# Kernel tuning notes

Measured on AMD Instinct MI355X. Metric: run time of the kernel, lower is better.

The kernel has to match this reference:

```python
import jax, jax.numpy as jnp
import numpy as np

B, S, D, MULT, K, EPS = 8, 2048, 512, 4, 9, 1e-6


def setup_inputs() -> dict:
    key = jax.random.key(0)
    ks = jax.random.split(key, 12)
    w = lambda k, shape, s=0.02: jax.random.normal(k, shape, dtype=jnp.float32) * s
    return dict(
        x=jax.random.normal(ks[0], (B, S, D), dtype=jnp.float32),
        g=jnp.ones((D,), jnp.float32),
        W1=w(ks[1], (D, D)), b1=jnp.zeros((D,), jnp.float32),
        W2=w(ks[2], (D, D)), b2=jnp.zeros((D,), jnp.float32),
        dw_w=w(ks[3], (D, D, K)), dw_b=jnp.zeros((D,), jnp.float32),
        pw_w=w(ks[4], (D, D, 1)), pw_b=jnp.zeros((D,), jnp.float32),
        Wi=w(ks[5], (D, D)), bi=jnp.zeros((D,), jnp.float32),
        Wr=w(ks[6], (D, D)), br=jnp.zeros((D,), jnp.float32),
        lam=jax.random.normal(ks[7], (D,), dtype=jnp.float32),
        Wm1=w(ks[8], (D, D * MULT)), bm1=jnp.zeros((D * MULT,), jnp.float32),
        Wm2=w(ks[9], (D * MULT, D)), bm2=jnp.zeros((D,), jnp.float32),
    )


def _rglru(x, Wi, bi, Wr, br, lam):
    # Griffin RG-LRU: h_t = a_t * h_{t-1} + sqrt(1 - a_t^2) * (i_t * x_t), h_0 = 0
    r = jax.nn.sigmoid(x @ Wr + br)                 # [B,S,D] recurrence gate
    i = jax.nn.sigmoid(x @ Wi + bi)                 # [B,S,D] input gate
    log_a = -8.0 * jax.nn.softplus(lam) * r         # [B,S,D]
    a = jnp.exp(log_a)
    b = jnp.sqrt(1.0 - jnp.exp(2.0 * log_a)) * (i * x)

    def combine(e1, e2):
        a1, b1 = e1
        a2, b2 = e2
        return (a1 * a2, a2 * b1 + b2)

    _, h = jax.lax.associative_scan(combine, (a, b), axis=1)
    return h


def _conv1d(x_cdS, w_oik, b_o, pad):
    y = jax.lax.conv_general_dilated(
        x_cdS, w_oik, window_strides=(1,), padding=[pad],
        dimension_numbers=("NCH", "OIH", "NCH"))
    return y + b_o[None, :, None]


def reference(x, g, W1, b1, W2, b2, dw_w, dw_b, pw_w, pw_b,
              Wi, bi, Wr, br, lam, Wm1, bm1, Wm2, bm2):
    scale = jnp.sqrt(jnp.float32(D))

    def rms(t):  # matches torch: x / (||x||_2 + eps) * sqrt(D) * g
        n = jnp.linalg.norm(t, axis=-1, keepdims=True) + EPS
        return t / n * scale * g

    skip = x
    xn = rms(x)
    l1 = xn @ W1 + b1                               # [B,S,D]
    l2 = xn @ W2 + b2                               # [B,S,D]
    c = jnp.transpose(l1, (0, 2, 1))                # [B,D,S]
    c = _conv1d(c, dw_w, dw_b, (K // 2, K // 2))    # 'same' padding, k=9
    c = _conv1d(c, pw_w, pw_b, (0, 0))              # pointwise k=1
    l1 = jnp.transpose(c, (0, 2, 1))                # [B,S,D]
    l1 = _rglru(l1, Wi, bi, Wr, br, lam)
    x1 = l1 * jax.nn.gelu(l2, approximate=False) + skip

    skip2 = x1
    xn2 = rms(x1)
    h = xn2 @ Wm1 + bm1                             # [B,S,4D]
    out = (jax.nn.gelu(h, approximate=False) * h) @ Wm2 + bm2 + skip2
    return out
```

## Files before the change

### kernel.cpp

```cpp
#include <hip/hip_runtime.h>
#include <hip/hip_bf16.h>

typedef unsigned short ushort_t;
typedef unsigned short vus8 __attribute__((ext_vector_type(8)));
typedef short vs8 __attribute__((ext_vector_type(8)));
typedef float vf4 __attribute__((ext_vector_type(4)));

#define D_DIM 512
#define S_LEN 2048
#define B_SZ 8
#define T_TOK 16384
#define NCH 64
#define CLEN 32

__device__ __forceinline__ float bf2f(ushort_t u) {
  union { unsigned int i; float f; } v;
  v.i = ((unsigned int)u) << 16;
  return v.f;
}
__device__ __forceinline__ ushort_t f2bf(float f) {
  union { float f; unsigned int i; } v;
  v.f = f;
  unsigned int r = v.i + 0x7fffu + ((v.i >> 16) & 1u);
  return (ushort_t)(r >> 16);
}
__device__ __forceinline__ float gelu_exact(float x) {
  return 0.5f * x * (1.0f + erff(x * 0.7071067811865475f));
}
__device__ __forceinline__ float ld_in(const void* p, size_t i, int fl) {
  return fl ? ((const float*)p)[i] : bf2f(((const ushort_t*)p)[i]);
}
__device__ __forceinline__ void gld_lds16(const ushort_t* g, ushort_t* l) {
  __builtin_amdgcn_global_load_lds(
      (const __attribute__((address_space(1))) unsigned int*)g,
      (__attribute__((address_space(3))) unsigned int*)l, 16, 0, 0);
}

__device__ __forceinline__ void ab_compute(ushort_t rp, ushort_t ip, ushort_t xv,
                                           float sp8, float& a, float& b) {
  float r = 1.f / (1.f + expf(-bf2f(rp)));
  float ig = 1.f / (1.f + expf(-bf2f(ip)));
  float la = -sp8 * r;
  a = expf(la);
  b = sqrtf(fmaxf(0.f, -expm1f(2.f * la))) * ig * bf2f(xv);
}

__global__ void detect_flag(const void* g, int* flag) {
  const ushort_t* u = (const ushort_t*)g;
  flag[0] = (u[0] == 0x3F80 && u[1] == 0x3F80) ? 0 : 1;
  flag[1] = 0;
}

#define NJOBS 18
struct PrepJobs {
  const void* src[NJOBS];
  ushort_t* dst[NJOBS];
  int R[NJOBS];
  int C[NJOBS];
  int mode[NJOBS];
  int start[NJOBS];
  int njobs;
};
__global__ void mega_prep(PrepJobs J, const int* __restrict__ flag) {
  __shared__ ushort_t ts[32][33];
  int fl = *flag;
  int bid = blockIdx.x;
  int j = 0;
  while (j + 1 < J.njobs && bid >= J.start[j + 1]) j++;
  int tile = bid - J.start[j];
  const void* in = J.src[j];
  ushort_t* out = J.dst[j];
  int mode = J.mode[j];
  if (mode == 2) {
    int n = J.R[j];
    int base = tile * 8192;
#pragma unroll 4
    for (int q = 0; q < 32; q++) {
      int i = base + q * 256 + threadIdx.x;
      if (i < n) out[i] = fl ? f2bf(((const float*)in)[i]) : ((const ushort_t*)in)[i];
    }
    return;
  }
  int R = J.R[j], C = J.C[j];
  int tpr = C >> 5;
  int bc = tile % tpr, br = tile / tpr;
  int tx = threadIdx.x & 31, ty = threadIdx.x >> 5;
#pragma unroll
  for (int i = 0; i < 32; i += 8) {
    size_t idx = (size_t)(br * 32 + ty + i) * C + bc * 32 + tx;
    ts[ty + i][tx] = fl ? f2bf(((const float*)in)[idx]) : ((const ushort_t*)in)[idx];
  }
  __syncthreads();
#pragma unroll
  for (int i = 0; i < 32; i += 8) {
    int r = bc * 32 + ty + i;
    int orow = (mode == 1) ? (r % 9) * 512 + r / 9 : r;
    out[(size_t)orow * R + br * 32 + tx] = ts[tx][ty + i];
  }
}

__global__ void gam_kernel(const ushort_t* __restrict__ tpw, const ushort_t* __restrict__ dwbc,
                           const ushort_t* __restrict__ pwbc, float* __restrict__ gam) {
  int wave = threadIdx.x >> 6, lane = threadIdx.x & 63;
  int o = blockIdx.x * 4 + wave;
  vus8 v = *(const vus8*)(tpw + (size_t)o * 512 + lane * 8);
  vus8 w = *(const vus8*)(dwbc + lane * 8);
  float p = 0.f;
#pragma unroll
  for (int q = 0; q < 8; q++) p += bf2f(v[q]) * bf2f(w[q]);
#pragma unroll
  for (int off = 32; off; off >>= 1) p += __shfl_xor(p, off, 64);
  if (lane == 0) gam[o] = p + bf2f(pwbc[o]);
}

__global__ void rms_kernel(const void* __restrict__ x, const int* __restrict__ flag,
                           const ushort_t* __restrict__ gc, ushort_t* __restrict__ out) {
  int fl = *flag;
  int wave = threadIdx.x >> 6, lane = threadIdx.x & 63;
  int row = blockIdx.x * 4 + wave;
  size_t base = (size_t)row * D_DIM + lane * 8;
  float f[8];
  float ss = 0.f;
#pragma unroll
  for (int j = 0; j < 8; j++) { f[j] = ld_in(x, base + j, fl); ss += f[j] * f[j]; }
#pragma unroll
  for (int off = 32; off > 0; off >>= 1) ss += __shfl_xor(ss, off, 64);
  float sc = 22.62741699796952f / (sqrtf(ss) + 1e-6f);
  vus8 o;
#pragma unroll
  for (int j = 0; j < 8; j++) o[j] = f2bf(f[j] * sc * bf2f(gc[lane * 8 + j]));
  *(vus8*)(out + base) = o;
}

template <int ACT>
__global__ __launch_bounds__(256, 2) void gemm_bt(
    const ushort_t* __restrict__ A, const ushort_t* __restrict__ Bt,
    const ushort_t* __restrict__ bias, void* __restrict__ Cv,
    const ushort_t* __restrict__ skip, const int* __restrict__ outflag, int N, int K, int lda,
    int row0, size_t zsA, size_t zsB, size_t zsC) {
  __shared__ __align__(16) ushort_t As[128 * 32];
  __shared__ __align__(16) ushort_t Bs[128 * 32];
  A += (size_t)blockIdx.z * zsA;
  Bt += (size_t)blockIdx.z * zsB;
  const size_t zC = (size_t)blockIdx.z * zsC;
  const int tid = threadIdx.x;
  const int bm = blockIdx.y, bn = blockIdx.x;
  const int wave = tid >> 6, lane = tid & 63;
  const int wm = wave & 1, wn = wave >> 1;
  const int quad = lane >> 4, l16 = lane & 15;
  const int ofl = (ACT == 2) ? *outflag : 0;
  const int srow = wave * 32 + (lane >> 2);
  const int scol = (lane & 3) * 8;
  const ushort_t* gA = A + (size_t)(bm * 128 + srow) * lda + scol;
  const ushort_t* gB = Bt + (size_t)(bn * 128 + srow) * K + scol;
  ushort_t* lA0 = As + (wave * 32) * 32;
  ushort_t* lA1 = As + (wave * 32 + 16) * 32;
  ushort_t* lB0 = Bs + (wave * 32) * 32;
  ushort_t* lB1 = Bs + (wave * 32 + 16) * 32;
  vf4 acc[4][4] = {};
  for (int k0 = 0; k0 < K; k0 += 32) {
    __syncthreads();
    gld_lds16(gA + k0, lA0);
    gld_lds16(gA + k0 + (size_t)16 * lda, lA1);
    gld_lds16(gB + k0, lB0);
    gld_lds16(gB + k0 + (size_t)16 * K, lB1);
    __syncthreads();
    vs8 af[4], bfr[4];
#pragma unroll
    for (int mi = 0; mi < 4; mi++)
      af[mi] = *(const vs8*)(As + (wm * 64 + mi * 16 + l16) * 32 + quad * 8);
#pragma unroll
    for (int ni = 0; ni < 4; ni++)
      bfr[ni] = *(const vs8*)(Bs + (wn * 64 + ni * 16 + l16) * 32 + quad * 8);
#pragma unroll
    for (int mi = 0; mi < 4; mi++)
#pragma unroll
      for (int ni = 0; ni < 4; ni++)
        acc[mi][ni] =
            __builtin_amdgcn_mfma_f32_16x16x32_bf16(af[mi], bfr[ni], acc[mi][ni], 0, 0, 0);
  }
#pragma unroll
  for (int mi = 0; mi < 4; mi++) {
#pragma unroll
    for (int ni = 0; ni < 4; ni++) {
      int gcol = bn * 128 + wn * 64 + ni * 16 + l16;
      float bv = bias ? bf2f(bias[gcol]) : 0.f;
#pragma unroll
      for (int r = 0; r < 4; r++) {
        int grow = row0 + bm * 128 + wm * 64 + mi * 16 + quad * 4 + r;
        size_t oidx = zC + (size_t)grow * N + gcol;
        float v = acc[mi][ni][r] + bv;
        if (ACT == 1) v = gelu_exact(v) * v;
        if (ACT == 2) v += bf2f(skip[(size_t)grow * N + gcol]);
        if (ACT == 2 && ofl) ((float*)Cv)[oidx] = v;
        else ((ushort_t*)Cv)[oidx] = f2bf(v);
      }
    }
  }
}

#define LDA_CONV 1024
__global__ __launch_bounds__(256, 2) void conv_gemm(
    const ushort_t* __restrict__ A, const ushort_t* __restrict__ Bt9,
    const float* __restrict__ gam, ushort_t* __restrict__ C) {
  __shared__ __align__(16) ushort_t Ah[136 * 32];
  __shared__ __align__(16) ushort_t Bs[3 * 128 * 32];
  const int tid = threadIdx.x;
  const int bid = blockIdx.x;
  const int xid = bid & 7, cid = bid >> 3;
  const int bn = xid >> 1;
  const int bm = (xid & 1) * 64 + cid;
  const int wave = tid >> 6, lane = tid & 63;
  const int wm = wave & 1, wn = wave >> 1;
  const int quad = lane >> 4, l16 = lane & 15;
  const int pos = bm & 15;
  const bool first = (pos == 0), last = (pos == 15);
  const int blrow = lane >> 2;
  const int bscol = (lane & 3) * 8;
  vf4 acc[4][4] = {};
  for (int k0 = 0; k0 < D_DIM; k0 += 32) {
    __syncthreads();
    for (int c = tid; c < 544; c += 256) {
      int j = c >> 2, col = (c & 3) * 8;
      vus8 v = {0, 0, 0, 0, 0, 0, 0, 0};
      bool valid = !((first && j < 4) || (last && j >= 132));
      if (valid)
        v = *(const vus8*)(A + (size_t)(bm * 128 + j - 4) * LDA_CONV + k0 + col);
      *(vus8*)(Ah + j * 32 + col) = v;
    }
#pragma unroll
    for (int kg = 0; kg < 3; kg++) {
      if (kg) __syncthreads();
#pragma unroll
      for (int h = 0; h < 6; h++) {
        int m = h * 4 + wave;
        int r = m * 16 + blrow;
        int kbl = m >> 3;
        int ro = r & 127;
        const ushort_t* g = Bt9 + ((size_t)(kg * 3 + kbl) * D_DIM + bn * 128 + ro) * D_DIM +
                            k0 + bscol;
        gld_lds16(g, Bs + m * 16 * 32);
      }
      __syncthreads();
#pragma unroll
      for (int kbl = 0; kbl < 3; kbl++) {
        int kb = kg * 3 + kbl;
        vs8 af[4], bfr[4];
#pragma unroll
        for (int mi = 0; mi < 4; mi++)
          af[mi] = *(const vs8*)(Ah + (wm * 64 + mi * 16 + l16 + kb) * 32 + quad * 8);
#pragma unroll
        for (int ni = 0; ni < 4; ni++)
          bfr[ni] = *(const vs8*)(Bs + kbl * 4096 + (wn * 64 + ni * 16 + l16) * 32 + quad * 8);
#pragma unroll
        for (int mi = 0; mi < 4; mi++)
#pragma unroll
          for (int ni = 0; ni < 4; ni++)
            acc[mi][ni] =
                __builtin_amdgcn_mfma_f32_16x16x32_bf16(af[mi], bfr[ni], acc[mi][ni], 0, 0, 0);
      }
    }
  }
#pragma unroll
  for (int mi = 0; mi < 4; mi++) {
#pragma unroll
    for (int ni = 0; ni < 4; ni++) {
      int gcol = bn * 128 + wn * 64 + ni * 16 + l16;
      float gv = gam[gcol];
#pragma unroll
      for (int r = 0; r < 4; r++) {
        int grow = bm * 128 + wm * 64 + mi * 16 + quad * 4 + r;
        C[(size_t)grow * D_DIM + gcol] = f2bf(acc[mi][ni][r] + gv);
      }
    }
  }
}

__global__ void scan_pass1(const ushort_t* __restrict__ P, const ushort_t* __restrict__ xin,
                           const ushort_t* __restrict__ lamc, float* __restrict__ Aagg,
                           float* __restrict__ Bagg) {
  int bid = blockIdx.x;
  int dblk = bid & 1, c = (bid >> 1) & (NCH - 1), bb = bid >> 7;
  int d = dblk * 256 + threadIdx.x;
  float l = bf2f(lamc[d]);
  float sp8 = 8.f * ((l > 20.f) ? l : log1pf(expf(l)));
  size_t baseP = ((size_t)bb * S_LEN + c * CLEN) * 1024 + d;
  size_t baseX = ((size_t)bb * S_LEN + c * CLEN) * D_DIM + d;
  float Ap = 1.f, h = 0.f;
  for (int s = 0; s < CLEN; s++) {
    float av, bv;
    ab_compute(P[baseP + (size_t)s * 1024], P[baseP + 512 + (size_t)s * 1024],
               xin[baseX + (size_t)s * D_DIM], sp8, av, bv);
    Ap *= av;
    h = av * h + bv;
  }
  size_t o = ((size_t)bb * NCH + c) * D_DIM + d;
  Aagg[o] = Ap;
  Bagg[o] = h;
}

__global__ void scan_carry(const float* __restrict__ Aagg, const float* __restrict__ Bagg,
                           float* __restrict__ carry) {
  int idx = blockIdx.x * 256 + threadIdx.x;
  int bb = idx >> 9, d = idx & (D_DIM - 1);
  float h = 0.f;
  for (int c = 0; c < NCH; c++) {
    size_t o = ((size_t)bb * NCH + c) * D_DIM + d;
    carry[o] = h;
    h = Aagg[o] * h + Bagg[o];
  }
}

__global__ void scan_pass2(const ushort_t* __restrict__ P, const ushort_t* xin,
                           const ushort_t* __restrict__ lamc, const float* __restrict__ carry,
                           const ushort_t* __restrict__ P12, const void* __restrict__ x,
                           const int* __restrict__ flag, ushort_t* x1) {
  int fl = *flag;
  int bid = blockIdx.x;
  int dblk = bid & 1, c = (bid >> 1) & (NCH - 1), bb = bid >> 7;
  int d = dblk * 256 + threadIdx.x;
  float l = bf2f(lamc[d]);
  float sp8 = 8.f * ((l > 20.f) ? l : log1pf(expf(l)));
  float h = carry[((size_t)bb * NCH + c) * D_DIM + d];
  size_t baseP = ((size_t)bb * S_LEN + c * CLEN) * 1024 + d;
  size_t baseL = ((size_t)bb * S_LEN + c * CLEN) * 1024 + 512 + d;
  size_t base = ((size_t)bb * S_LEN + c * CLEN) * D_DIM + d;
  for (int s = 0; s < CLEN; s++) {
    size_t idx = base + (size_t)s * D_DIM;
    float av, bv;
    ab_compute(P[baseP + (size_t)s * 1024], P[baseP + 512 + (size_t)s * 1024], xin[idx], sp8,
               av, bv);
    h = av * h + bv;
    float l2v = bf2f(P12[baseL + (size_t)s * 1024]);
    float xv = ld_in(x, idx, fl);
    x1[idx] = f2bf(h * gelu_exact(l2v) + xv);
  }
}

extern "C" void kernel_launch(void* const* d_in, const int* in_sizes, int n_in, void* d_out,
                              int out_size, void* d_ws, size_t ws_size, hipStream_t stream) {
  (void)in_sizes; (void)n_in; (void)out_size; (void)ws_size;
  const void* x   = d_in[0];
  const void* g   = d_in[1];
  const void* W1  = d_in[2];
  const void* b1  = d_in[3];
  const void* W2  = d_in[4];
  const void* b2  = d_in[5];
  const void* dww = d_in[6];
  const void* dwb = d_in[7];
  const void* pww = d_in[8];
  const void* pwb = d_in[9];
  const void* Wi  = d_in[10];
  const void* bi  = d_in[11];
  const void* Wr  = d_in[12];
  const void* br  = d_in[13];
  const void* lam = d_in[14];
  const void* Wm1 = d_in[15];
  const void* bm1 = d_in[16];
  const void* Wm2 = d_in[17];
  const void* bm2 = d_in[18];

  char* ws = (char*)d_ws;
  size_t off = 0;
  auto take = [&](size_t n) {
    void* p = ws + off;
    off += (n + 255) & ~(size_t)255;
    return p;
  };
  const size_t ACT_B = (size_t)T_TOK * D_DIM * 2;
  int* flag = (int*)take(256);
  ushort_t* tW12 = (ushort_t*)take((size_t)1024 * 512 * 2);
  ushort_t* tWri = (ushort_t*)take((size_t)1024 * 512 * 2);
  ushort_t* tWm1 = (ushort_t*)take((size_t)2048 * 512 * 2);
  ushort_t* tWm2 = (ushort_t*)take((size_t)2048 * 512 * 2);
  ushort_t* Wp   = (ushort_t*)take((size_t)9 * 512 * 512 * 2);
  ushort_t* gc   = (ushort_t*)take(512 * 2);
  ushort_t* lamc = (ushort_t*)take(512 * 2);
  ushort_t* b12c = (ushort_t*)take(1024 * 2);
  ushort_t* bric = (ushort_t*)take(1024 * 2);
  ushort_t* bm2c = (ushort_t*)take(512 * 2);
  ushort_t* bm1c = (ushort_t*)take(2048 * 2);
  ushort_t* dwbc = (ushort_t*)take(512 * 2);
  ushort_t* pwbc = (ushort_t*)take(512 * 2);
  float* gam     = (float*)take(512 * 4);
  ushort_t* S0 = (ushort_t*)take(ACT_B);
  ushort_t* S1 = (ushort_t*)take(ACT_B);
  ushort_t* S2 = (ushort_t*)take(ACT_B);
  ushort_t* S3 = (ushort_t*)take(ACT_B);
  ushort_t* S4 = (ushort_t*)take(ACT_B);
  float* Aagg  = (float*)take((size_t)B_SZ * NCH * D_DIM * 4);
  float* Bagg  = (float*)take((size_t)B_SZ * NCH * D_DIM * 4);
  float* carry = (float*)take((size_t)B_SZ * NCH * D_DIM * 4);
  const int* zflag = flag + 1;
  ushort_t* tpw  = S2;
  ushort_t* tdwT = S3;
  ushort_t* P12  = S0;
  ushort_t* Pri  = S3;
  ushort_t* u2   = S0;

  detect_flag<<<1, 1, 0, stream>>>(g, flag);
  PrepJobs J;
  const void* js[NJOBS] = {g, lam, b1, b2, dwb, pwb, br, bi, bm2, bm1, pww,
                           W1, W2, Wr, Wi, Wm1, Wm2, dww};
  ushort_t* jd[NJOBS] = {gc, lamc, b12c, b12c + 512, dwbc, pwbc, bric, bric + 512, bm2c, bm1c,
                         tpw, tW12, tW12 + (size_t)512 * 512, tWri, tWri + (size_t)512 * 512,
                         tWm1, tWm2, tdwT};
  int jR[NJOBS] = {512, 512, 512, 512, 512, 512, 512, 512, 512, 2048, 262144,
                   512, 512, 512, 512, 512, 2048, 512};
  int jC[NJOBS] = {0, 0, 0, 0, 0, 0, 0, 0, 0, 0, 0, 512, 512, 512, 512, 2048, 512, 4608};
  int jm[NJOBS] = {2, 2, 2, 2, 2, 2, 2, 2, 2, 2, 2, 0, 0, 0, 0, 0, 0, 1};
  int cum = 0;
  for (int i = 0; i < NJOBS; i++) {
    J.src[i] = js[i]; J.dst[i] = jd[i]; J.R[i] = jR[i]; J.C[i] = jC[i]; J.mode[i] = jm[i];
    J.start[i] = cum;
    cum += (jm[i] == 2) ? (jR[i] + 8191) / 8192 : (jC[i] / 32) * (jR[i] / 32);
  }
  J.njobs = NJOBS;
  mega_prep<<<cum, 256, 0, stream>>>(J, flag);
  gemm_bt<0><<<dim3(4, 4, 9), 256, 0, stream>>>(tpw, tdwT, nullptr, Wp, nullptr, zflag, 512,
                                                512, 512, 0, 0, (size_t)512 * 512,
                                                (size_t)512 * 512);
  gam_kernel<<<128, 256, 0, stream>>>(tpw, dwbc, pwbc, gam);

  rms_kernel<<<T_TOK / 4, 256, 0, stream>>>(x, flag, gc, S4);
  gemm_bt<0><<<dim3(8, 128), 256, 0, stream>>>(S4, tW12, b12c, P12, nullptr, zflag, 1024, 512,
                                               512, 0, 0, 0, 0);
  conv_gemm<<<512, 256, 0, stream>>>(P12, Wp, gam, S2);
  gemm_bt<0><<<dim3(8, 128), 256, 0, stream>>>(S2, tWri, bric, Pri, nullptr, zflag, 1024, 512,
                                               512, 0, 0, 0, 0);
  scan_pass1<<<B_SZ * NCH * 2, 256, 0, stream>>>(Pri, S2, lamc, Aagg, Bagg);
  scan_carry<<<16, 256, 0, stream>>>(Aagg, Bagg, carry);
  scan_pass2<<<B_SZ * NCH * 2, 256, 0, stream>>>(Pri, S2, lamc, carry, P12, x, flag, S2);

  rms_kernel<<<T_TOK / 4, 256, 0, stream>>>(S2, zflag, gc, S4);
  for (int c = 0; c < 2; c++) {
    const ushort_t* xc = S4 + (size_t)c * 8192 * D_DIM;
    gemm_bt<1><<<dim3(16, 64), 256, 0, stream>>>(xc, tWm1, bm1c, u2, nullptr, zflag, 2048, 512,
                                                 512, 0, 0, 0, 0);
    gemm_bt<2><<<dim3(4, 64), 256, 0, stream>>>(u2, tWm2, bm2c, d_out, S2, flag, 512, 2048,
                                                2048, c * 8192, 0, 0, 0);
  }
}
```

Before: 566.2 us.

## Fold second RMSNorm into MLP GEMM epilogue and drop flag kernel

Removes the second rms_kernel pass. Row sum-of-squares is now accumulated with atomics inside scan_pass2, the gain vector is folded into Wm1 during weight prep, and the per-row scale is applied in a new GEMM epilogue before the GELU. It also drops the detect_flag launch by checking the input dtype inline, precomputes the softplus of lam once, and runs the MLP as two full-size GEMMs instead of two chunks. The cost is a memset plus per-row atomics in the scan, and applying the norm after the bf16 matmul rather than before it changes rounding slightly.

```diff
diff --git a/kernel.cpp b/kernel.cpp
--- a/kernel.cpp
+++ b/kernel.cpp
@@ -29,6 +29,9 @@
 }
 __device__ __forceinline__ float ld_in(const void* p, size_t i, int fl) {
   return fl ? ((const float*)p)[i] : bf2f(((const ushort_t*)p)[i]);
+}
+__device__ __forceinline__ int dt_fl(const ushort_t* gdt) {
+  return !(gdt[0] == 0x3F80 && gdt[1] == 0x3F80);
 }
 __device__ __forceinline__ void gld_lds16(const ushort_t* g, ushort_t* l) {
   __builtin_amdgcn_global_load_lds(
@@ -43,12 +46,6 @@
   float la = -sp8 * r;
   a = expf(la);
   b = sqrtf(fmaxf(0.f, -expm1f(2.f * la))) * ig * bf2f(xv);
-}
-
-__global__ void detect_flag(const void* g, int* flag) {
-  const ushort_t* u = (const ushort_t*)g;
-  flag[0] = (u[0] == 0x3F80 && u[1] == 0x3F80) ? 0 : 1;
-  flag[1] = 0;
 }
 
 #define NJOBS 18
@@ -59,11 +56,12 @@
   int C[NJOBS];
   int mode[NJOBS];
   int start[NJOBS];
+  const void* gsrc;
   int njobs;
 };
-__global__ void mega_prep(PrepJobs J, const int* __restrict__ flag) {
+__global__ void mega_prep(PrepJobs J, const ushort_t* __restrict__ gdt) {
   __shared__ ushort_t ts[32][33];
-  int fl = *flag;
+  int fl = dt_fl(gdt);
   int bid = blockIdx.x;
   int j = 0;
   while (j + 1 < J.njobs && bid >= J.start[j + 1]) j++;
@@ -95,12 +93,23 @@
   for (int i = 0; i < 32; i += 8) {
     int r = bc * 32 + ty + i;
     int orow = (mode == 1) ? (r % 9) * 512 + r / 9 : r;
-    out[(size_t)orow * R + br * 32 + tx] = ts[tx][ty + i];
+    ushort_t val = ts[tx][ty + i];
+    if (mode == 3) {
+      int kcol = br * 32 + tx;
+      val = f2bf(bf2f(val) * ld_in(J.gsrc, kcol, fl));
+    }
+    out[(size_t)orow * R + br * 32 + tx] = val;
   }
 }
 
 __global__ void gam_kernel(const ushort_t* __restrict__ tpw, const ushort_t* __restrict__ dwbc,
-                           const ushort_t* __restrict__ pwbc, float* __restrict__ gam) {
+                           const ushort_t* __restrict__ pwbc, const ushort_t* __restrict__ lamc,
+                           float* __restrict__ gam, float* __restrict__ sp8b) {
+  int t = blockIdx.x * 256 + threadIdx.x;
+  if (t < 512) {
+    float l = bf2f(lamc[t]);
+    sp8b[t] = 8.f * ((l > 20.f) ? l : log1pf(expf(l)));
+  }
   int wave = threadIdx.x >> 6, lane = threadIdx.x & 63;
   int o = blockIdx.x * 4 + wave;
   vus8 v = *(const vus8*)(tpw + (size_t)o * 512 + lane * 8);
@@ -113,9 +122,9 @@
   if (lane == 0) gam[o] = p + bf2f(pwbc[o]);
 }
 
-__global__ void rms_kernel(const void* __restrict__ x, const int* __restrict__ flag,
+__global__ void rms_kernel(const void* __restrict__ x, const ushort_t* __restrict__ gdt,
                            const ushort_t* __restrict__ gc, ushort_t* __restrict__ out) {
-  int fl = *flag;
+  int fl = dt_fl(gdt);
   int wave = threadIdx.x >> 6, lane = threadIdx.x & 63;
   int row = blockIdx.x * 4 + wave;
   size_t base = (size_t)row * D_DIM + lane * 8;
@@ -136,8 +145,9 @@
 __global__ __launch_bounds__(256, 2) void gemm_bt(
     const ushort_t* __restrict__ A, const ushort_t* __restrict__ Bt,
     const ushort_t* __restrict__ bias, void* __restrict__ Cv,
-    const ushort_t* __restrict__ skip, const int* __restrict__ outflag, int N, int K, int lda,
-    int row0, size_t zsA, size_t zsB, size_t zsC) {
+    const ushort_t* __restrict__ skip, const float* __restrict__ rowss,
+    const ushort_t* __restrict__ gdt, int N, int K, int lda, int row0,
+    size_t zsA, size_t zsB, size_t zsC) {
   __shared__ __align__(16) ushort_t As[128 * 32];
   __shared__ __align__(16) ushort_t Bs[128 * 32];
   A += (size_t)blockIdx.z * zsA;
@@ -148,7 +158,7 @@
   const int wave = tid >> 6, lane = tid & 63;
   const int wm = wave & 1, wn = wave >> 1;
   const int quad = lane >> 4, l16 = lane & 15;
-  const int ofl = (ACT == 2) ? *outflag : 0;
+  const int ofl = (ACT == 2) ? dt_fl(gdt) : 0;
   const int srow = wave * 32 + (lane >> 2);
   const int scol = (lane & 3) * 8;
   const ushort_t* gA = A + (size_t)(bm * 128 + srow) * lda + scol;
@@ -189,8 +199,14 @@
       for (int r = 0; r < 4; r++) {
         int grow = row0 + bm * 128 + wm * 64 + mi * 16 + quad * 4 + r;
         size_t oidx = zC + (size_t)grow * N + gcol;
-        float v = acc[mi][ni][r] + bv;
-        if (ACT == 1) v = gelu_exact(v) * v;
+        float v;
+        if (ACT == 3) {
+          float sc = 22.62741699796952f / (sqrtf(rowss[grow]) + 1e-6f);
+          v = acc[mi][ni][r] * sc + bv;
+          v = gelu_exact(v) * v;
+        } else {
+          v = acc[mi][ni][r] + bv;
+        }
         if (ACT == 2) v += bf2f(skip[(size_t)grow * N + gcol]);
         if (ACT == 2 && ofl) ((float*)Cv)[oidx] = v;
         else ((ushort_t*)Cv)[oidx] = f2bf(v);
@@ -277,13 +293,12 @@
 }
 
 __global__ void scan_pass1(const ushort_t* __restrict__ P, const ushort_t* __restrict__ xin,
-                           const ushort_t* __restrict__ lamc, float* __restrict__ Aagg,
+                           const float* __restrict__ sp8b, float* __restrict__ Aagg,
                            float* __restrict__ Bagg) {
   int bid = blockIdx.x;
   int dblk = bid & 1, c = (bid >> 1) & (NCH - 1), bb = bid >> 7;
   int d = dblk * 256 + threadIdx.x;
-  float l = bf2f(lamc[d]);
-  float sp8 = 8.f * ((l > 20.f) ? l : log1pf(expf(l)));
+  float sp8 = sp8b[d];
   size_t baseP = ((size_t)bb * S_LEN + c * CLEN) * 1024 + d;
   size_t baseX = ((size_t)bb * S_LEN + c * CLEN) * D_DIM + d;
   float Ap = 1.f, h = 0.f;
@@ -311,29 +326,35 @@
   }
 }
 
-__global__ void scan_pass2(const ushort_t* __restrict__ P, const ushort_t* xin,
-                           const ushort_t* __restrict__ lamc, const float* __restrict__ carry,
-                           const ushort_t* __restrict__ P12, const void* __restrict__ x,
-                           const int* __restrict__ flag, ushort_t* x1) {
-  int fl = *flag;
+__global__ void scan_pass2(const ushort_t* __restrict__ P, const float* __restrict__ sp8b,
+                           const float* __restrict__ carry, const ushort_t* __restrict__ P12,
+                           const void* __restrict__ x, const ushort_t* __restrict__ gdt,
+                           ushort_t* xio, float* __restrict__ rowss) {
+  int fl = dt_fl(gdt);
   int bid = blockIdx.x;
   int dblk = bid & 1, c = (bid >> 1) & (NCH - 1), bb = bid >> 7;
   int d = dblk * 256 + threadIdx.x;
-  float l = bf2f(lamc[d]);
-  float sp8 = 8.f * ((l > 20.f) ? l : log1pf(expf(l)));
+  int lane = threadIdx.x & 63;
+  float sp8 = sp8b[d];
   float h = carry[((size_t)bb * NCH + c) * D_DIM + d];
   size_t baseP = ((size_t)bb * S_LEN + c * CLEN) * 1024 + d;
   size_t baseL = ((size_t)bb * S_LEN + c * CLEN) * 1024 + 512 + d;
   size_t base = ((size_t)bb * S_LEN + c * CLEN) * D_DIM + d;
+  int row0 = bb * S_LEN + c * CLEN;
   for (int s = 0; s < CLEN; s++) {
     size_t idx = base + (size_t)s * D_DIM;
     float av, bv;
-    ab_compute(P[baseP + (size_t)s * 1024], P[baseP + 512 + (size_t)s * 1024], xin[idx], sp8,
+    ab_compute(P[baseP + (size_t)s * 1024], P[baseP + 512 + (size_t)s * 1024], xio[idx], sp8,
                av, bv);
     h = av * h + bv;
     float l2v = bf2f(P12[baseL + (size_t)s * 1024]);
     float xv = ld_in(x, idx, fl);
-    x1[idx] = f2bf(h * gelu_exact(l2v) + xv);
+    float v = h * gelu_exact(l2v) + xv;
+    xio[idx] = f2bf(v);
+    float p = v * v;
+#pragma unroll
+    for (int o2 = 32; o2; o2 >>= 1) p += __shfl_xor(p, o2, 64);
+    if (lane == 0) atomicAdd(&rowss[row0 + s], p);
   }
 }
 
@@ -359,6 +380,7 @@
   const void* bm1 = d_in[16];
   const void* Wm2 = d_in[17];
   const void* bm2 = d_in[18];
+  const ushort_t* gdt = (const ushort_t*)g;
 
   char* ws = (char*)d_ws;
   size_t off = 0;
@@ -368,7 +390,6 @@
     return p;
   };
   const size_t ACT_B = (size_t)T_TOK * D_DIM * 2;
-  int* flag = (int*)take(256);
   ushort_t* tW12 = (ushort_t*)take((size_t)1024 * 512 * 2);
   ushort_t* tWri = (ushort_t*)take((size_t)1024 * 512 * 2);
   ushort_t* tWm1 = (ushort_t*)take((size_t)2048 * 512 * 2);
@@ -383,6 +404,8 @@
   ushort_t* dwbc = (ushort_t*)take(512 * 2);
   ushort_t* pwbc = (ushort_t*)take(512 * 2);
   float* gam     = (float*)take(512 * 4);
+  float* sp8b    = (float*)take(512 * 4);
+  float* rowss   = (float*)take((size_t)T_TOK * 4);
   ushort_t* S0 = (ushort_t*)take(ACT_B);
   ushort_t* S1 = (ushort_t*)take(ACT_B);
   ushort_t* S2 = (ushort_t*)take(ACT_B);
@@ -391,14 +414,14 @@
   float* Aagg  = (float*)take((size_t)B_SZ * NCH * D_DIM * 4);
   float* Bagg  = (float*)take((size_t)B_SZ * NCH * D_DIM * 4);
   float* carry = (float*)take((size_t)B_SZ * NCH * D_DIM * 4);
-  const int* zflag = flag + 1;
-  ushort_t* tpw  = S2;
-  ushort_t* tdwT = S3;
-  ushort_t* P12  = S0;
-  ushort_t* Pri  = S3;
-  ushort_t* u2   = S0;
-
-  detect_flag<<<1, 1, 0, stream>>>(g, flag);
+  ushort_t* tpw  = S0;
+  ushort_t* tdwT = S1;
+  ushort_t* Pri  = S0;
+  ushort_t* P12  = S2;
+  ushort_t* u    = S0;
+
+  hipMemsetAsync(rowss, 0, (size_t)T_TOK * 4, stream);
+
   PrepJobs J;
   const void* js[NJOBS] = {g, lam, b1, b2, dwb, pwb, br, bi, bm2, bm1, pww,
                            W1, W2, Wr, Wi, Wm1, Wm2, dww};
@@ -408,36 +431,33 @@
   int jR[NJOBS] = {512, 512, 512, 512, 512, 512, 512, 512, 512, 2048, 262144,
                    512, 512, 512, 512, 512, 2048, 512};
   int jC[NJOBS] = {0, 0, 0, 0, 0, 0, 0, 0, 0, 0, 0, 512, 512, 512, 512, 2048, 512, 4608};
-  int jm[NJOBS] = {2, 2, 2, 2, 2, 2, 2, 2, 2, 2, 2, 0, 0, 0, 0, 0, 0, 1};
+  int jm[NJOBS] = {2, 2, 2, 2, 2, 2, 2, 2, 2, 2, 2, 0, 0, 0, 0, 3, 0, 1};
   int cum = 0;
   for (int i = 0; i < NJOBS; i++) {
     J.src[i] = js[i]; J.dst[i] = jd[i]; J.R[i] = jR[i]; J.C[i] = jC[i]; J.mode[i] = jm[i];
     J.start[i] = cum;
     cum += (jm[i] == 2) ? (jR[i] + 8191) / 8192 : (jC[i] / 32) * (jR[i] / 32);
   }
+  J.gsrc = g;
   J.njobs = NJOBS;
-  mega_prep<<<cum, 256, 0, stream>>>(J, flag);
-  gemm_bt<0><<<dim3(4, 4, 9), 256, 0, stream>>>(tpw, tdwT, nullptr, Wp, nullptr, zflag, 512,
-                                                512, 512, 0, 0, (size_t)512 * 512,
+  mega_prep<<<cum, 256, 0, stream>>>(J, gdt);
+  gemm_bt<0><<<dim3(4, 4, 9), 256, 0, stream>>>(tpw, tdwT, nullptr, Wp, nullptr, nullptr, gdt,
+                                                512, 512, 512, 0, 0, (size_t)512 * 512,
                                                 (size_t)512 * 512);
-  gam_kernel<<<128, 256, 0, stream>>>(tpw, dwbc, pwbc, gam);
-
-  rms_kernel<<<T_TOK / 4, 256, 0, stream>>>(x, flag, gc, S4);
-  gemm_bt<0><<<dim3(8, 128), 256, 0, stream>>>(S4, tW12, b12c, P12, nullptr, zflag, 1024, 512,
-                                               512, 0, 0, 0, 0);
-  conv_gemm<<<512, 256, 0, stream>>>(P12, Wp, gam, S2);
-  gemm_bt<0><<<dim3(8, 128), 256, 0, stream>>>(S2, tWri, bric, Pri, nullptr, zflag, 1024, 512,
-                                               512, 0, 0, 0, 0);
-  scan_pass1<<<B_SZ * NCH * 2, 256, 0, stream>>>(Pri, S2, lamc, Aagg, Bagg);
+  gam_kernel<<<128, 256, 0, stream>>>(tpw, dwbc, pwbc, lamc, gam, sp8b);
+
+  rms_kernel<<<T_TOK / 4, 256, 0, stream>>>(x, gdt, gc, S4);
+  gemm_bt<0><<<dim3(8, 128), 256, 0, stream>>>(S4, tW12, b12c, P12, nullptr, nullptr, gdt,
+                                               1024, 512, 512, 0, 0, 0, 0);
+  conv_gemm<<<512, 256, 0, stream>>>(P12, Wp, gam, S4);
+  gemm_bt<0><<<dim3(8, 128), 256, 0, stream>>>(S4, tWri, bric, Pri, nullptr, nullptr, gdt,
+                                               1024, 512, 512, 0, 0, 0, 0);
+  scan_pass1<<<B_SZ * NCH * 2, 256, 0, stream>>>(Pri, S4, sp8b, Aagg, Bagg);
   scan_carry<<<16, 256, 0, stream>>>(Aagg, Bagg, carry);
-  scan_pass2<<<B_SZ * NCH * 2, 256, 0, stream>>>(Pri, S2, lamc, carry, P12, x, flag, S2);
-
-  rms_kernel<<<T_TOK / 4, 256, 0, stream>>>(S2, zflag, gc, S4);
-  for (int c = 0; c < 2; c++) {
-    const ushort_t* xc = S4 + (size_t)c * 8192 * D_DIM;
-    gemm_bt<1><<<dim3(16, 64), 256, 0, stream>>>(xc, tWm1, bm1c, u2, nullptr, zflag, 2048, 512,
-                                                 512, 0, 0, 0, 0);
-    gemm_bt<2><<<dim3(4, 64), 256, 0, stream>>>(u2, tWm2, bm2c, d_out, S2, flag, 512, 2048,
-                                                2048, c * 8192, 0, 0, 0);
-  }
-}
+  scan_pass2<<<B_SZ * NCH * 2, 256, 0, stream>>>(Pri, sp8b, carry, P12, x, gdt, S4, rowss);
+
+  gemm_bt<3><<<dim3(16, 128), 256, 0, stream>>>(S4, tWm1, bm1c, u, nullptr, rowss, gdt, 2048,
+                                                512, 512, 0, 0, 0, 0);
+  gemm_bt<2><<<dim3(4, 128), 256, 0, stream>>>(u, tWm2, bm2c, d_out, S4, nullptr, gdt, 512,
+                                               2048, 2048, 0, 0, 0, 0);
+}
```

Result: faster. 517.9 us (-8.5%).
